# Kernel tuning notes

Measured on AMD Instinct MI355X. Metric: run time of the kernel, lower is better.

## Reference

```python
import jax, jax.numpy as jnp
import numpy as np
from jax import lax

DIM = 1024      # model dim
DS = 16         # d_state
DC = 4          # d_conv
EXP = 2
DI = DIM * EXP  # d_inner = 2048
B, L = 2, 1024


def setup_inputs() -> dict:
    key = jax.random.key(0)
    ks = jax.random.split(key, 10)
    s = lambda k, shape, sc: jax.random.normal(k, shape, jnp.float32) * sc
    return {
        "x": s(ks[0], (B, L, DIM), 1.0),
        "norm_w": jnp.ones((DIM,), jnp.float32),
        "norm_b": jnp.zeros((DIM,), jnp.float32),
        "in_proj_w": s(ks[1], (2 * DI, DIM), DIM ** -0.5),
        "conv_w": s(ks[2], (DI, 1, DC), DC ** -0.5),   # depthwise: (out=DI, in/groups=1, K)
        "conv_b": jnp.zeros((DI,), jnp.float32),
        "x_proj_w": s(ks[3], (2 * DS + 1, DI), DI ** -0.5),
        "dt_w": s(ks[4], (DI, 1), 1.0),
        "dt_b": jax.random.uniform(ks[5], (DI,), jnp.float32, -0.001, 0.001),
        "A_log": s(ks[6], (DI, DS), 1.0),              # self.A (randn); A = -exp(A_log)
        "D_skip": jnp.ones((DI,), jnp.float32),
        "out_proj_w": s(ks[7], (DIM, DI), DI ** -0.5),
    }


def _ssm(x, x_proj_w, dt_w, dt_b, A_log, D_skip):
    # x: (B, L, DI)
    xp = jnp.einsum('bli,pi->blp', x, x_proj_w)            # (B, L, 2*DS+1)
    delta = jax.nn.softplus(xp[..., :1] * dt_w[:, 0] + dt_b)  # (B, L, DI)
    Bp = xp[..., 1:DS + 1]                                  # (B, L, DS)
    Cp = xp[..., DS + 1:]                                   # (B, L, DS)
    A = -jnp.exp(A_log)                                     # (DI, DS)
    dA = jnp.exp(delta[..., None] * A)                      # (B, L, DI, DS)
    dB = delta[..., None] * Bp[:, :, None, :] * x[..., None]  # (B, L, DI, DS)

    def step(h, inp):
        dA_t, dB_t, C_t = inp                               # (B,DI,DS),(B,DI,DS),(B,DS)
        h = dA_t * h + dB_t
        return h, jnp.einsum('bdn,bn->bd', h, C_t)

    h0 = jnp.zeros((x.shape[0], DI, DS), x.dtype)
    _, ys = lax.scan(step, h0, (jnp.swapaxes(dA, 0, 1),
                                jnp.swapaxes(dB, 0, 1),
                                jnp.swapaxes(Cp, 0, 1)))
    y = jnp.swapaxes(ys, 0, 1)                              # (B, L, DI)
    return y + x * D_skip


def reference(x, norm_w, norm_b, in_proj_w, conv_w, conv_b,
              x_proj_w, dt_w, dt_b, A_log, D_skip, out_proj_w):
    # LayerNorm
    mu = x.mean(-1, keepdims=True)
    var = ((x - mu) ** 2).mean(-1, keepdims=True)
    xn = (x - mu) * lax.rsqrt(var + 1e-5) * norm_w + norm_b
    # input projection and gate split
    xz = jnp.einsum('bld,pd->blp', xn, in_proj_w)           # (B, L, 2*DI)
    xi, z = xz[..., :DI], xz[..., DI:]
    # causal depthwise conv (torch pads K-1 both sides then slices [:L] == left-pad K-1)
    xc = lax.conv_general_dilated(jnp.swapaxes(xi, 1, 2), conv_w, (1,),
                                  [(DC - 1, 0)], feature_group_count=DI,
                                  dimension_numbers=('NCH', 'OIH', 'NCH'))
    xc = jnp.swapaxes(xc + conv_b[None, :, None], 1, 2)     # (B, L, DI)
    xc = jax.nn.silu(xc)
    y = _ssm(xc, x_proj_w, dt_w, dt_b, A_log, D_skip)
    y = y * jax.nn.silu(z)
    return x + jnp.einsum('bli,di->bld', y, out_proj_w)
```

## Files before the change

kernel.cpp:

```cpp
#include <hip/hip_runtime.h>
#include <stdint.h>

#define BATCH 2
#define SEQ   1024
#define DIM_  1024
#define DS_   16
#define DI_   2048
#define NTOK  (BATCH*SEQ)
#define NSEG  32
#define LSEG  (SEQ/NSEG)

typedef unsigned short u16;
using s16x8 = __attribute__((ext_vector_type(8))) short;
using f32x4 = __attribute__((ext_vector_type(4))) float;
using u16x4 = __attribute__((ext_vector_type(4))) unsigned short;
using u16x8 = __attribute__((ext_vector_type(8))) unsigned short;

__device__ __forceinline__ float bf2f(u16 u) {
  union { unsigned int i; float f; } c; c.i = ((unsigned int)u) << 16; return c.f;
}
__device__ __forceinline__ u16 f2bf(float f) {
  union { float f; unsigned int i; } c; c.f = f;
  unsigned int r = c.i + 0x7fffu + ((c.i >> 16) & 1u);
  return (u16)(r >> 16);
}
__device__ __forceinline__ float softplus_f(float x) {
  return (x > 15.f) ? x : __logf(1.f + __expf(x));
}
__device__ __forceinline__ u16x4 f4_to_bf(float4 v) {
  u16x4 r; r[0] = f2bf(v.x); r[1] = f2bf(v.y); r[2] = f2bf(v.z); r[3] = f2bf(v.w);
  return r;
}

#define N4_INW  (2 * DI_ * DIM_ / 4)
#define N4_OUTW (DIM_ * DI_ / 4)
#define CVT_BLOCKS ((N4_INW + N4_OUTW + 32768) / 256)
__global__ __launch_bounds__(256) void cvt_ln_kernel(const float* __restrict__ in_w,
    const float* __restrict__ out_w, const float* __restrict__ xproj_w,
    const float* __restrict__ x, const float* __restrict__ nw,
    const float* __restrict__ nb, u16* __restrict__ in_w_bf,
    u16* __restrict__ out_w_bf, u16* __restrict__ xpw_bf, u16* __restrict__ xn) {
  int tid = threadIdx.x;
  if (blockIdx.x < CVT_BLOCKS) {
    int i = blockIdx.x * 256 + tid;
    if (i < N4_INW) {
      ((u16x4*)in_w_bf)[i] = f4_to_bf(((const float4*)in_w)[i]);
    } else if (i < N4_INW + N4_OUTW) {
      int j = i - N4_INW;
      ((u16x4*)out_w_bf)[j] = f4_to_bf(((const float4*)out_w)[j]);
    } else {
      int j = i - (N4_INW + N4_OUTW);
      if (j >= 32768) return;
      int p = (j * 4) >> 11;
      u16x4 r;
      if (p < 33) r = f4_to_bf(((const float4*)xproj_w)[j]);
      else { r[0] = 0; r[1] = 0; r[2] = 0; r[3] = 0; }
      ((u16x4*)xpw_bf)[j] = r;
    }
    return;
  }
  int t = blockIdx.x - CVT_BLOCKS;
  const float* row = x + (size_t)t * DIM_;
  float4 v = ((const float4*)row)[tid];
  float f[4] = {v.x, v.y, v.z, v.w};
  float s = 0.f, sq = 0.f;
#pragma unroll
  for (int j = 0; j < 4; j++) { s += f[j]; sq += f[j] * f[j]; }
#pragma unroll
  for (int m = 1; m < 64; m <<= 1) { s += __shfl_xor(s, m); sq += __shfl_xor(sq, m); }
  __shared__ float rs_[4], rq_[4];
  int wv = tid >> 6;
  if ((tid & 63) == 0) { rs_[wv] = s; rq_[wv] = sq; }
  __syncthreads();
  s = rs_[0] + rs_[1] + rs_[2] + rs_[3];
  sq = rq_[0] + rq_[1] + rq_[2] + rq_[3];
  float mu = s * (1.0f / DIM_);
  float var = sq * (1.0f / DIM_) - mu * mu;
  float rstd = rsqrtf(var + 1e-5f);
  float4 wn = ((const float4*)nw)[tid];
  float4 bn = ((const float4*)nb)[tid];
  u16x4 o;
  o[0] = f2bf((f[0] - mu) * rstd * wn.x + bn.x);
  o[1] = f2bf((f[1] - mu) * rstd * wn.y + bn.y);
  o[2] = f2bf((f[2] - mu) * rstd * wn.z + bn.z);
  o[3] = f2bf((f[3] - mu) * rstd * wn.w + bn.w);
  *(u16x4*)(xn + (size_t)t * DIM_ + tid * 4) = o;
}

template<int TBM, int TBN, int BK, typename OUT, int EPI, int KSPLIT = 1, int SWZ = 0>
__global__ __launch_bounds__(256) void gemm_bt(const u16* __restrict__ A,
    const u16* __restrict__ Wt, OUT* __restrict__ C, const float* __restrict__ X,
    int M, int N, int K) {
  constexpr int LDT = BK + 8;
  constexpr int TPR = BK / 8;
  constexpr int RPP = 256 / TPR;
  constexpr int ALn = TBM / RPP;
  constexpr int BLn = TBN / RPP;
  constexpr int KK = BK / 32;
  constexpr int WM = TBM / 2, WN = TBN / 2;
  constexpr int MI = WM / 16, NJ = WN / 16;
  __shared__ __align__(16) u16 sA[TBM * LDT];
  __shared__ __align__(16) u16 sB[TBN * LDT];
  const int tid = threadIdx.x;
  const int lane = tid & 63, wv = tid >> 6;
  const int wm = (wv >> 1) * WM, wn = (wv & 1) * WN;
  const int bxl = SWZ ? ((blockIdx.x & 7) * (gridDim.x >> 3) + (blockIdx.x >> 3))
                      : blockIdx.x;
  const int bm0 = blockIdx.y * TBM, bn0 = bxl * TBN;
  const int q = lane >> 4, r16 = lane & 15;
  const int srow = tid / TPR, scol = (tid % TPR) * 8;
  const int kc = K / KSPLIT;
  const int k0 = (KSPLIT > 1) ? blockIdx.z * kc : 0;
  const int kend = k0 + kc;

  f32x4 acc[MI][NJ];
#pragma unroll
  for (int i = 0; i < MI; i++)
#pragma unroll
    for (int j = 0; j < NJ; j++)
#pragma unroll
      for (int r = 0; r < 4; r++) acc[i][j][r] = 0.f;

  const u16* Ag = A + (size_t)bm0 * K + scol + k0;
  const u16* Wg = Wt + (size_t)bn0 * K + scol + k0;
  s16x8 ra[ALn], rb[BLn];
#pragma unroll
  for (int i = 0; i < ALn; i++) ra[i] = *(const s16x8*)(Ag + (size_t)(srow + i * RPP) * K);
#pragma unroll
  for (int i = 0; i < BLn; i++) rb[i] = *(const s16x8*)(Wg + (size_t)(srow + i * RPP) * K);

  for (int kt = k0; kt < kend; kt += BK) {
    __syncthreads();
#pragma unroll
    for (int i = 0; i < ALn; i++) *(s16x8*)&sA[(srow + i * RPP) * LDT + scol] = ra[i];
#pragma unroll
    for (int i = 0; i < BLn; i++) *(s16x8*)&sB[(srow + i * RPP) * LDT + scol] = rb[i];
    __syncthreads();
    int kn = kt + BK - k0;
    if (kn < kc) {
#pragma unroll
      for (int i = 0; i < ALn; i++) ra[i] = *(const s16x8*)(Ag + (size_t)(srow + i * RPP) * K + kn);
#pragma unroll
      for (int i = 0; i < BLn; i++) rb[i] = *(const s16x8*)(Wg + (size_t)(srow + i * RPP) * K + kn);
    }
#pragma unroll
    for (int kk = 0; kk < KK; kk++) {
      s16x8 fa[MI], fb[NJ];
#pragma unroll
      for (int i = 0; i < MI; i++)
        fa[i] = *(const s16x8*)&sA[(wm + i * 16 + r16) * LDT + kk * 32 + q * 8];
#pragma unroll
      for (int j = 0; j < NJ; j++)
        fb[j] = *(const s16x8*)&sB[(wn + j * 16 + r16) * LDT + kk * 32 + q * 8];
#pragma unroll
      for (int i = 0; i < MI; i++)
#pragma unroll
        for (int j = 0; j < NJ; j++)
          acc[i][j] = __builtin_amdgcn_mfma_f32_16x16x32_bf16(fa[i], fb[j], acc[i][j], 0, 0, 0);
    }
  }
  OUT* Cz = C + ((KSPLIT > 1) ? (size_t)blockIdx.z * M * N : 0);
#pragma unroll
  for (int i = 0; i < MI; i++)
#pragma unroll
    for (int j = 0; j < NJ; j++) {
      int row0 = bm0 + wm + i * 16 + q * 4;
      int col = bn0 + wn + j * 16 + r16;
#pragma unroll
      for (int r = 0; r < 4; r++) {
        size_t off = (size_t)(row0 + r) * N + col;
        float v = acc[i][j][r];
        if constexpr (EPI == 1) v += X[off];
        if constexpr (sizeof(OUT) == 2) Cz[off] = f2bf(v);
        else                            Cz[off] = v;
      }
    }
}

__global__ __launch_bounds__(256) void convxp_gemm(const u16* __restrict__ xz,
    const float* __restrict__ cw, const float* __restrict__ cb,
    const u16* __restrict__ Wt, float* __restrict__ C, u16* __restrict__ xc) {
  constexpr int BK = 32, LDT = BK + 8;
  constexpr int WM = 32, WN = 32, MI = 2, NJ = 2;
  constexpr int K = DI_, Nn = 64;
  __shared__ __align__(16) u16 sA[64 * LDT];
  __shared__ __align__(16) u16 sB[64 * LDT];
  const int tid = threadIdx.x;
  const int lane = tid & 63, wv = tid >> 6;
  const int wm = (wv >> 1) * WM, wn = (wv & 1) * WN;
  const int bm0 = blockIdx.y * 64;
  const int q = lane >> 4, r16 = lane & 15;
  const int srow = tid >> 2, scol = (tid & 3) * 8;
  const int kc = K / 8;
  const int k0 = blockIdx.z * kc;

  f32x4 acc[MI][NJ];
#pragma unroll
  for (int i = 0; i < MI; i++)
#pragma unroll
    for (int j = 0; j < NJ; j++)
#pragma unroll
      for (int r = 0; r < 4; r++) acc[i][j][r] = 0.f;

  const int tm = bm0 + srow;
  const int l = tm & (SEQ - 1);
  const u16* Wg = Wt + (size_t)srow * K + scol + k0;

  auto conv8 = [&](int kt) -> s16x8 {
    int ch = k0 + kt + scol;
    float a[8];
    float4 cb0 = *(const float4*)(cb + ch);
    float4 cb1 = *(const float4*)(cb + ch + 4);
    a[0] = cb0.x; a[1] = cb0.y; a[2] = cb0.z; a[3] = cb0.w;
    a[4] = cb1.x; a[5] = cb1.y; a[6] = cb1.z; a[7] = cb1.w;
#pragma unroll
    for (int k = 0; k < 4; k++) {
      if (l - 3 + k >= 0) {
        u16x8 v = *(const u16x8*)(xz + (size_t)(tm - 3 + k) * (2 * DI_) + ch);
#pragma unroll
        for (int j = 0; j < 8; j++) {
          float4 wj = ((const float4*)cw)[ch + j];
          float wk = (k == 0) ? wj.x : (k == 1) ? wj.y : (k == 2) ? wj.z : wj.w;
          a[j] = fmaf(bf2f(v[j]), wk, a[j]);
        }
      }
    }
    u16x8 o;
#pragma unroll
    for (int j = 0; j < 8; j++) {
      float s = a[j] / (1.0f + __expf(-a[j]));
      o[j] = f2bf(s);
    }
    *(u16x8*)(xc + (size_t)tm * DI_ + ch) = o;
    return *(s16x8*)&o;
  };

  s16x8 ra = conv8(0);
  s16x8 rb = *(const s16x8*)Wg;

  for (int kt = 0; kt < kc; kt += BK) {
    __syncthreads();
    *(s16x8*)&sA[srow * LDT + scol] = ra;
    *(s16x8*)&sB[srow * LDT + scol] = rb;
    __syncthreads();
    int kn = kt + BK;
    if (kn < kc) {
      ra = conv8(kn);
      rb = *(const s16x8*)(Wg + kn);
    }
    {
      s16x8 fa[MI], fb[NJ];
#pragma unroll
      for (int i = 0; i < MI; i++)
        fa[i] = *(const s16x8*)&sA[(wm + i * 16 + r16) * LDT + q * 8];
#pragma unroll
      for (int j = 0; j < NJ; j++)
        fb[j] = *(const s16x8*)&sB[(wn + j * 16 + r16) * LDT + q * 8];
#pragma unroll
      for (int i = 0; i < MI; i++)
#pragma unroll
        for (int j = 0; j < NJ; j++)
          acc[i][j] = __builtin_amdgcn_mfma_f32_16x16x32_bf16(fa[i], fb[j], acc[i][j], 0, 0, 0);
    }
  }
  float* Cz = C + (size_t)blockIdx.z * NTOK * Nn;
#pragma unroll
  for (int i = 0; i < MI; i++)
#pragma unroll
    for (int j = 0; j < NJ; j++) {
      int row0 = bm0 + wm + i * 16 + q * 4;
      int col = wn + j * 16 + r16;
#pragma unroll
      for (int r = 0; r < 4; r++)
        Cz[(size_t)(row0 + r) * Nn + col] = acc[i][j][r];
    }
}

__global__ __launch_bounds__(256) void xp_finish_kernel(const float* __restrict__ part,
    const float* __restrict__ dtw, const float* __restrict__ dtb,
    u16* __restrict__ xz, float* __restrict__ bc) {
  int t = blockIdx.x;
  int tid = threadIdx.x;
  __shared__ float xps[64];
  if (tid < 64) {
    float s = 0.f;
#pragma unroll
    for (int k = 0; k < 8; k++)
      s += part[(size_t)k * NTOK * 64 + (size_t)t * 64 + tid];
    xps[tid] = s;
  }
  __syncthreads();
  if (tid < 32) bc[(size_t)t * 32 + tid] = xps[1 + tid];
  float dr = xps[0];
  int c0 = tid * 8;
  float wv[8], bv[8];
  *(float4*)wv = ((const float4*)(dtw + c0))[0];
  *(float4*)(wv + 4) = ((const float4*)(dtw + c0))[1];
  *(float4*)bv = ((const float4*)(dtb + c0))[0];
  *(float4*)(bv + 4) = ((const float4*)(dtb + c0))[1];
  u16x8 o;
#pragma unroll
  for (int j = 0; j < 8; j++) o[j] = f2bf(softplus_f(dr * wv[j] + bv[j]));
  *(u16x8*)(xz + (size_t)t * (2 * DI_) + c0) = o;
}

#define SRT 72
#define SBC 36

__global__ __launch_bounds__(256) void scan_pass1(const float* __restrict__ bc,
    const u16* __restrict__ dlt, const u16* __restrict__ xc,
    const float* __restrict__ A_log, float* __restrict__ P, float* __restrict__ Q) {
  __shared__ __align__(16) u16 sD[LSEG * SRT];
  __shared__ __align__(16) u16 sX[LSEG * SRT];
  __shared__ __align__(16) float sB[LSEG * SBC];
  int tid = threadIdx.x;
  int lane = tid & 63, wv = tid >> 6;
  int nl = (lane & 3) * 4;
  int dl = wv * 16 + (lane >> 2);
  int d0 = blockIdx.x * 64;
  int s = blockIdx.y, b = blockIdx.z;
  int t0 = b * SEQ + s * LSEG;
  {
    int tr = tid >> 3, c = (tid & 7) * 8;
    *(u16x8*)&sD[tr * SRT + c] = *(const u16x8*)(dlt + (size_t)(t0 + tr) * (2 * DI_) + d0 + c);
    *(u16x8*)&sX[tr * SRT + c] = *(const u16x8*)(xc  + (size_t)(t0 + tr) * DI_ + d0 + c);
    int tb = tid & 31, cb = (tid >> 5) * 4;
    *(f32x4*)&sB[tb * SBC + cb] = *(const f32x4*)(bc + (size_t)(t0 + tb) * 32 + cb);
  }
  int d = d0 + dl;
  float4 Ain = *(const float4*)(A_log + d * DS_ + nl);
  f32x4 Av;
  Av[0] = -__expf(Ain.x); Av[1] = -__expf(Ain.y);
  Av[2] = -__expf(Ain.z); Av[3] = -__expf(Ain.w);
  f32x4 Pv, h;
#pragma unroll
  for (int i = 0; i < 4; i++) { Pv[i] = 1.f; h[i] = 0.f; }
  __syncthreads();
#pragma unroll 8
  for (int j = 0; j < LSEG; j++) {
    float delta = bf2f(sD[j * SRT + dl]);
    float xcv   = bf2f(sX[j * SRT + dl]);
    f32x4 B4 = *(const f32x4*)&sB[j * SBC + nl];
    float du = delta * xcv;
#pragma unroll
    for (int i = 0; i < 4; i++) {
      float a = __expf(delta * Av[i]);
      Pv[i] *= a;
      h[i] = fmaf(a, h[i], du * B4[i]);
    }
  }
  size_t idx = ((size_t)((b * NSEG + s) * DI_ + d)) * 16 + nl;
  *(f32x4*)(P + idx) = Pv;
  *(f32x4*)(Q + idx) = h;
}

__global__ __launch_bounds__(256) void scan_pass2(const float* __restrict__ bc,
    const u16* __restrict__ dlt, const u16* __restrict__ xc,
    const float* __restrict__ A_log, const float* __restrict__ Dskip,
    const float* __restrict__ P, const float* __restrict__ Q,
    u16* __restrict__ yb) {
  __shared__ __align__(16) u16 sD[LSEG * SRT];
  __shared__ __align__(16) u16 sX[LSEG * SRT];
  __shared__ __align__(16) u16 sZ[LSEG * SRT];
  __shared__ __align__(16) float sB[LSEG * SBC];
  int tid = threadIdx.x;
  int lane = tid & 63, wv = tid >> 6;
  int nl = (lane & 3) * 4;
  int dl = wv * 16 + (lane >> 2);
  int d0 = blockIdx.x * 64;
  int s = blockIdx.y, b = blockIdx.z;
  int t0 = b * SEQ + s * LSEG;
  {
    int tr = tid >> 3, c = (tid & 7) * 8;
    *(u16x8*)&sD[tr * SRT + c] = *(const u16x8*)(dlt + (size_t)(t0 + tr) * (2 * DI_) + d0 + c);
    *(u16x8*)&sZ[tr * SRT + c] = *(const u16x8*)(dlt + (size_t)(t0 + tr) * (2 * DI_) + DI_ + d0 + c);
    *(u16x8*)&sX[tr * SRT + c] = *(const u16x8*)(xc  + (size_t)(t0 + tr) * DI_ + d0 + c);
    int tb = tid & 31, cb = (tid >> 5) * 4;
    *(f32x4*)&sB[tb * SBC + cb] = *(const f32x4*)(bc + (size_t)(t0 + tb) * 32 + cb);
  }
  int d = d0 + dl;
  float4 Ain = *(const float4*)(A_log + d * DS_ + nl);
  f32x4 Av;
  Av[0] = -__expf(Ain.x); Av[1] = -__expf(Ain.y);
  Av[2] = -__expf(Ain.z); Av[3] = -__expf(Ain.w);
  float Dv = Dskip[d];
  f32x4 h;
#pragma unroll
  for (int i = 0; i < 4; i++) h[i] = 0.f;
  for (int s2 = 0; s2 < s; s2++) {
    size_t ix = ((size_t)((b * NSEG + s2) * DI_ + d)) * 16 + nl;
    f32x4 Pv = *(const f32x4*)(P + ix);
    f32x4 Qv = *(const f32x4*)(Q + ix);
#pragma unroll
    for (int i = 0; i < 4; i++) h[i] = fmaf(Pv[i], h[i], Qv[i]);
  }
  __syncthreads();
#pragma unroll 8
  for (int j = 0; j < LSEG; j++) {
    float delta = bf2f(sD[j * SRT + dl]);
    float xcv   = bf2f(sX[j * SRT + dl]);
    f32x4 B4 = *(const f32x4*)&sB[j * SBC + nl];
    f32x4 C4 = *(const f32x4*)&sB[j * SBC + 16 + nl];
    float du = delta * xcv;
#pragma unroll
    for (int i = 0; i < 4; i++) {
      float a = __expf(delta * Av[i]);
      h[i] = fmaf(a, h[i], du * B4[i]);
    }
    float p = h[0] * C4[0];
    p = fmaf(h[1], C4[1], p);
    p = fmaf(h[2], C4[2], p);
    p = fmaf(h[3], C4[3], p);
    p += __shfl_xor(p, 1);
    p += __shfl_xor(p, 2);
    if ((lane & 3) == 0) {
      float z = bf2f(sZ[j * SRT + dl]);
      float sz = z / (1.0f + __expf(-z));
      yb[(size_t)(t0 + j) * DI_ + d] = f2bf((p + xcv * Dv) * sz);
    }
  }
}

extern "C" void kernel_launch(void* const* d_in, const int* in_sizes, int n_in,
                              void* d_out, int out_size, void* d_ws, size_t ws_size,
                              hipStream_t stream) {
  const float* x      = (const float*)d_in[0];
  const float* norm_w = (const float*)d_in[1];
  const float* norm_b = (const float*)d_in[2];
  const float* in_w   = (const float*)d_in[3];
  const float* conv_w = (const float*)d_in[4];
  const float* conv_b = (const float*)d_in[5];
  const float* xproj_w= (const float*)d_in[6];
  const float* dt_w   = (const float*)d_in[7];
  const float* dt_b   = (const float*)d_in[8];
  const float* A_log  = (const float*)d_in[9];
  const float* D_skip = (const float*)d_in[10];
  const float* out_w  = (const float*)d_in[11];
  float* out = (float*)d_out;

  char* ws = (char*)d_ws;
  size_t off = 0;
  auto alloc = [&](size_t bytes) { void* p = ws + off; off += (bytes + 255) & ~255ULL; return p; };
  u16* in_w_bf  = (u16*)alloc((size_t)2 * DI_ * DIM_ * 2);
  u16* out_w_bf = (u16*)alloc((size_t)DIM_ * DI_ * 2);
  u16* xpw_bf   = (u16*)alloc((size_t)64 * DI_ * 2);
  u16* xn       = (u16*)alloc((size_t)NTOK * DIM_ * 2);
  u16* xz       = (u16*)alloc((size_t)NTOK * 2 * DI_ * 2);
  u16* xc       = (u16*)alloc((size_t)NTOK * DI_ * 2);
  float* bc     = (float*)alloc((size_t)NTOK * 32 * 4);
  float* xp_part= (float*)alloc((size_t)8 * NTOK * 64 * 4);
  float* P      = (float*)alloc((size_t)BATCH * NSEG * DI_ * 16 * 4);
  float* Q      = (float*)alloc((size_t)BATCH * NSEG * DI_ * 16 * 4);
  u16* yb       = (u16*)alloc((size_t)NTOK * DI_ * 2);

  cvt_ln_kernel<<<CVT_BLOCKS + NTOK, 256, 0, stream>>>(in_w, out_w, xproj_w, x,
                                                       norm_w, norm_b, in_w_bf,
                                                       out_w_bf, xpw_bf, xn);
  gemm_bt<128, 128, 64, u16, 0, 1, 1><<<dim3((2 * DI_) / 128, NTOK / 128), 256, 0, stream>>>(
      xn, in_w_bf, xz, nullptr, NTOK, 2 * DI_, DIM_);
  convxp_gemm<<<dim3(1, NTOK / 64, 8), 256, 0, stream>>>(
      xz, conv_w, conv_b, xpw_bf, xp_part, xc);
  xp_finish_kernel<<<NTOK, 256, 0, stream>>>(xp_part, dt_w, dt_b, xz, bc);
  scan_pass1<<<dim3(DI_ / 64, NSEG, BATCH), 256, 0, stream>>>(bc, xz, xc, A_log, P, Q);
  scan_pass2<<<dim3(DI_ / 64, NSEG, BATCH), 256, 0, stream>>>(bc, xz, xc, A_log, D_skip,
                                                              P, Q, yb);
  gemm_bt<64, 64, 64, float, 1, 1, 1><<<dim3(DIM_ / 64, NTOK / 64), 256, 0, stream>>>(
      yb, out_w_bf, out, x, NTOK, DIM_, DI_);
}
```

Before: 217.9 us.

## Fuse xp_finish into convxp split-K GEMM via last-block atomic reduction

Removes the separate xp_finish kernel launch by having the last of the 8 split-K blocks per 64-token tile (found with an atomic counter and threadfence) reduce the partials and compute the softplus delta and B/C outputs. Delta now goes to a separate compact buffer instead of overwriting the xi half of xz, so the scan kernels read it from the new buffer. This saves one launch and its global round trip. In exchange, the delta computation is serialized onto 32 last blocks, each looping over 64 tokens, which lowers parallelism for that stage.

```diff
diff --git a/kernel.cpp b/kernel.cpp
--- a/kernel.cpp
+++ b/kernel.cpp
@@ -39,8 +39,10 @@
     const float* __restrict__ out_w, const float* __restrict__ xproj_w,
     const float* __restrict__ x, const float* __restrict__ nw,
     const float* __restrict__ nb, u16* __restrict__ in_w_bf,
-    u16* __restrict__ out_w_bf, u16* __restrict__ xpw_bf, u16* __restrict__ xn) {
+    u16* __restrict__ out_w_bf, u16* __restrict__ xpw_bf, u16* __restrict__ xn,
+    unsigned int* __restrict__ cnt) {
   int tid = threadIdx.x;
+  if (blockIdx.x == 0 && tid < NTOK / 64) cnt[tid] = 0;
   if (blockIdx.x < CVT_BLOCKS) {
     int i = blockIdx.x * 256 + tid;
     if (i < N4_INW) {
@@ -179,7 +181,9 @@
 
 __global__ __launch_bounds__(256) void convxp_gemm(const u16* __restrict__ xz,
     const float* __restrict__ cw, const float* __restrict__ cb,
-    const u16* __restrict__ Wt, float* __restrict__ C, u16* __restrict__ xc) {
+    const u16* __restrict__ Wt, float* __restrict__ C, u16* __restrict__ xc,
+    const float* __restrict__ dtw, const float* __restrict__ dtb,
+    float* __restrict__ bc, u16* __restrict__ dlt, unsigned int* __restrict__ cnt) {
   constexpr int BK = 32, LDT = BK + 8;
   constexpr int WM = 32, WN = 32, MI = 2, NJ = 2;
   constexpr int K = DI_, Nn = 64;
@@ -274,34 +278,46 @@
       for (int r = 0; r < 4; r++)
         Cz[(size_t)(row0 + r) * Nn + col] = acc[i][j][r];
     }
-}
-
-__global__ __launch_bounds__(256) void xp_finish_kernel(const float* __restrict__ part,
-    const float* __restrict__ dtw, const float* __restrict__ dtb,
-    u16* __restrict__ xz, float* __restrict__ bc) {
-  int t = blockIdx.x;
-  int tid = threadIdx.x;
-  __shared__ float xps[64];
-  if (tid < 64) {
+
+  __shared__ unsigned int isLast;
+  __threadfence();
+  if (tid == 0) {
+    unsigned int old = atomicAdd(&cnt[blockIdx.y], 1u);
+    isLast = (old == 7u) ? 1u : 0u;
+  }
+  __syncthreads();
+  if (!isLast) return;
+  __threadfence();
+
+  __shared__ float xps[64][33];
+  for (int idx = tid; idx < 64 * 33; idx += 256) {
+    int t = idx / 33, c = idx - t * 33;
     float s = 0.f;
 #pragma unroll
     for (int k = 0; k < 8; k++)
-      s += part[(size_t)k * NTOK * 64 + (size_t)t * 64 + tid];
-    xps[tid] = s;
+      s += C[(size_t)k * NTOK * 64 + (size_t)(bm0 + t) * 64 + c];
+    xps[t][c] = s;
   }
   __syncthreads();
-  if (tid < 32) bc[(size_t)t * 32 + tid] = xps[1 + tid];
-  float dr = xps[0];
-  int c0 = tid * 8;
-  float wv[8], bv[8];
-  *(float4*)wv = ((const float4*)(dtw + c0))[0];
-  *(float4*)(wv + 4) = ((const float4*)(dtw + c0))[1];
-  *(float4*)bv = ((const float4*)(dtb + c0))[0];
-  *(float4*)(bv + 4) = ((const float4*)(dtb + c0))[1];
-  u16x8 o;
-#pragma unroll
-  for (int j = 0; j < 8; j++) o[j] = f2bf(softplus_f(dr * wv[j] + bv[j]));
-  *(u16x8*)(xz + (size_t)t * (2 * DI_) + c0) = o;
+  for (int idx = tid; idx < 64 * 32; idx += 256) {
+    int t = idx >> 5, c = idx & 31;
+    bc[(size_t)(bm0 + t) * 32 + c] = xps[t][1 + c];
+  }
+  {
+    int c0 = tid * 8;
+    float wv8[8], bv8[8];
+    *(float4*)wv8       = ((const float4*)(dtw + c0))[0];
+    *(float4*)(wv8 + 4) = ((const float4*)(dtw + c0))[1];
+    *(float4*)bv8       = ((const float4*)(dtb + c0))[0];
+    *(float4*)(bv8 + 4) = ((const float4*)(dtb + c0))[1];
+    for (int t = 0; t < 64; t++) {
+      float dr = xps[t][0];
+      u16x8 o;
+#pragma unroll
+      for (int j = 0; j < 8; j++) o[j] = f2bf(softplus_f(dr * wv8[j] + bv8[j]));
+      *(u16x8*)(dlt + (size_t)(bm0 + t) * DI_ + c0) = o;
+    }
+  }
 }
 
 #define SRT 72
@@ -322,7 +338,7 @@
   int t0 = b * SEQ + s * LSEG;
   {
     int tr = tid >> 3, c = (tid & 7) * 8;
-    *(u16x8*)&sD[tr * SRT + c] = *(const u16x8*)(dlt + (size_t)(t0 + tr) * (2 * DI_) + d0 + c);
+    *(u16x8*)&sD[tr * SRT + c] = *(const u16x8*)(dlt + (size_t)(t0 + tr) * DI_ + d0 + c);
     *(u16x8*)&sX[tr * SRT + c] = *(const u16x8*)(xc  + (size_t)(t0 + tr) * DI_ + d0 + c);
     int tb = tid & 31, cb = (tid >> 5) * 4;
     *(f32x4*)&sB[tb * SBC + cb] = *(const f32x4*)(bc + (size_t)(t0 + tb) * 32 + cb);
@@ -355,7 +371,8 @@
 }
 
 __global__ __launch_bounds__(256) void scan_pass2(const float* __restrict__ bc,
-    const u16* __restrict__ dlt, const u16* __restrict__ xc,
+    const u16* __restrict__ dlt, const u16* __restrict__ xz,
+    const u16* __restrict__ xc,
     const float* __restrict__ A_log, const float* __restrict__ Dskip,
     const float* __restrict__ P, const float* __restrict__ Q,
     u16* __restrict__ yb) {
@@ -372,8 +389,8 @@
   int t0 = b * SEQ + s * LSEG;
   {
     int tr = tid >> 3, c = (tid & 7) * 8;
-    *(u16x8*)&sD[tr * SRT + c] = *(const u16x8*)(dlt + (size_t)(t0 + tr) * (2 * DI_) + d0 + c);
-    *(u16x8*)&sZ[tr * SRT + c] = *(const u16x8*)(dlt + (size_t)(t0 + tr) * (2 * DI_) + DI_ + d0 + c);
+    *(u16x8*)&sD[tr * SRT + c] = *(const u16x8*)(dlt + (size_t)(t0 + tr) * DI_ + d0 + c);
+    *(u16x8*)&sZ[tr * SRT + c] = *(const u16x8*)(xz + (size_t)(t0 + tr) * (2 * DI_) + DI_ + d0 + c);
     *(u16x8*)&sX[tr * SRT + c] = *(const u16x8*)(xc  + (size_t)(t0 + tr) * DI_ + d0 + c);
     int tb = tid & 31, cb = (tid >> 5) * 4;
     *(f32x4*)&sB[tb * SBC + cb] = *(const f32x4*)(bc + (size_t)(t0 + tb) * 32 + cb);
@@ -447,23 +464,24 @@
   u16* xn       = (u16*)alloc((size_t)NTOK * DIM_ * 2);
   u16* xz       = (u16*)alloc((size_t)NTOK * 2 * DI_ * 2);
   u16* xc       = (u16*)alloc((size_t)NTOK * DI_ * 2);
+  u16* dlt      = (u16*)alloc((size_t)NTOK * DI_ * 2);
   float* bc     = (float*)alloc((size_t)NTOK * 32 * 4);
   float* xp_part= (float*)alloc((size_t)8 * NTOK * 64 * 4);
   float* P      = (float*)alloc((size_t)BATCH * NSEG * DI_ * 16 * 4);
   float* Q      = (float*)alloc((size_t)BATCH * NSEG * DI_ * 16 * 4);
   u16* yb       = (u16*)alloc((size_t)NTOK * DI_ * 2);
+  unsigned int* cnt = (unsigned int*)alloc((size_t)(NTOK / 64) * 4);
 
   cvt_ln_kernel<<<CVT_BLOCKS + NTOK, 256, 0, stream>>>(in_w, out_w, xproj_w, x,
                                                        norm_w, norm_b, in_w_bf,
-                                                       out_w_bf, xpw_bf, xn);
+                                                       out_w_bf, xpw_bf, xn, cnt);
   gemm_bt<128, 128, 64, u16, 0, 1, 1><<<dim3((2 * DI_) / 128, NTOK / 128), 256, 0, stream>>>(
       xn, in_w_bf, xz, nullptr, NTOK, 2 * DI_, DIM_);
   convxp_gemm<<<dim3(1, NTOK / 64, 8), 256, 0, stream>>>(
-      xz, conv_w, conv_b, xpw_bf, xp_part, xc);
-  xp_finish_kernel<<<NTOK, 256, 0, stream>>>(xp_part, dt_w, dt_b, xz, bc);
-  scan_pass1<<<dim3(DI_ / 64, NSEG, BATCH), 256, 0, stream>>>(bc, xz, xc, A_log, P, Q);
-  scan_pass2<<<dim3(DI_ / 64, NSEG, BATCH), 256, 0, stream>>>(bc, xz, xc, A_log, D_skip,
-                                                              P, Q, yb);
+      xz, conv_w, conv_b, xpw_bf, xp_part, xc, dt_w, dt_b, bc, dlt, cnt);
+  scan_pass1<<<dim3(DI_ / 64, NSEG, BATCH), 256, 0, stream>>>(bc, dlt, xc, A_log, P, Q);
+  scan_pass2<<<dim3(DI_ / 64, NSEG, BATCH), 256, 0, stream>>>(bc, dlt, xz, xc, A_log,
+                                                              D_skip, P, Q, yb);
   gemm_bt<64, 64, 64, float, 1, 1, 1><<<dim3(DIM_ / 64, NTOK / 64), 256, 0, stream>>>(
       yb, out_w_bf, out, x, NTOK, DIM_, DI_);
 }
```

Result: slower. 263.0 us (+20.7%).
